# Performance work log

Hardware: AMD Instinct MI355X
Metric: run time of the kernel (lower is better)

Reference implementation:

```python
import jax, jax.numpy as jnp
import numpy as np

B, T, D, M, L = 4, 2048, 256, 128, 16
P = M * L  # max_pair_cnt


def setup_inputs() -> dict:
    key = jax.random.key(0)
    ks = jax.random.split(key, 11)
    head = jax.random.normal(ks[0], (B, P, T), jnp.float32) * 0.05
    tail = jax.random.normal(ks[1], (B, P, T), jnp.float32) * 0.05
    x = jax.random.normal(ks[2], (B, T, D), jnp.float32)
    coref_mention_position = jax.random.uniform(ks[3], (B, M, T), jnp.float32)
    lab = jax.random.uniform(ks[4], (B, P, 2), jnp.float32) + 1e-3
    coref_label = lab / lab.sum(-1, keepdims=True)  # already-softmaxed target
    coref_label_mask = jax.random.randint(ks[5], (B, P), 0, 2).astype(bool)
    lens = jnp.full((B, M), L, jnp.int32)  # uniform segment lengths
    w1 = jax.random.normal(ks[6], (3 * D, D), jnp.float32) / np.sqrt(3 * D).astype(np.float32)
    b1 = jnp.zeros((D,), jnp.float32)
    w2 = jax.random.normal(ks[7], (D, 2), jnp.float32) / np.sqrt(D).astype(np.float32)
    b2 = jnp.zeros((2,), jnp.float32)
    return {"head": head, "tail": tail, "lens": lens, "x": x,
            "coref_mention_position": coref_mention_position,
            "coref_label": coref_label, "coref_label_mask": coref_label_mask,
            "w1": w1, "b1": b1, "w2": w2, "b2": b2}


def reference(head, tail, lens, x, coref_mention_position, coref_label,
              coref_label_mask, w1, b1, w2, b2):
    # bmm-based gather of mention reps: [B,P,T] @ [B,T,D] -> [B,P,D]
    head_rep = jnp.einsum('bpt,btd->bpd', head, x)
    tail_rep = jnp.einsum('bpt,btd->bpd', tail, x)
    feat = jnp.concatenate([head_rep, tail_rep, head_rep * tail_rep], axis=-1)
    logits = jax.nn.relu(feat @ w1 + b1) @ w2 + b2  # [B,P,2]

    # ragged split_n_pad -> per-mention top-1 select (uniform lens == L -> reshape)
    scores = logits[..., 1].reshape(B, M, L)            # [B,M,L]
    max_idx = jnp.argmax(scores, axis=-1)               # [B,M]
    max_val = jnp.max(scores, axis=-1)                  # [B,M] (raw logit, as in source)
    tail_seg = tail_rep.reshape(B, M, L, D)
    sel = jnp.take_along_axis(tail_seg, max_idx[:, :, None, None], axis=2)[:, :, 0, :]
    coref_rep_m = sel * max_val[:, :, None]             # [B,M,D]

    # scatter-bmm merge back into sequence: [B,T,M] @ [B,M,D] -> [B,T,D]
    coref_rep = jnp.einsum('bmt,bmd->btd', coref_mention_position, coref_rep_m)
    output = x + coref_rep

    # KLDivLoss(reduction='mean') over masked pairs
    logq = jax.nn.log_softmax(logits, axis=-1)
    lab = coref_label
    pw = jnp.where(lab > 0, lab * jnp.log(jnp.maximum(lab, 1e-38)), 0.0) - lab * logq
    n = jnp.sum(coref_label_mask).astype(jnp.float32)
    loss = jnp.where(coref_label_mask[..., None], pw, 0.0).sum() / (n * 2.0)
    return output, loss
```

## Files before the change

### kernel.cpp

```cpp
#include <hip/hip_runtime.h>
#include <hip/hip_bf16.h>
#include <stdint.h>

#define TAU 0.05f

typedef __attribute__((ext_vector_type(8))) _Float16 f16x8;
typedef __attribute__((ext_vector_type(4))) float f32x4;

__device__ __forceinline__ unsigned short f2h(float f) {
  _Float16 h = (_Float16)f;
  return __builtin_bit_cast(unsigned short, h);
}
__device__ __forceinline__ void async_copy16(const void* g, void* l) {
  __builtin_amdgcn_global_load_lds(
      (const __attribute__((address_space(1))) unsigned int*)g,
      (__attribute__((address_space(3))) unsigned int*)l, 16, 0, 0);
}

__global__ __launch_bounds__(256) void k_prep(
    const float* __restrict__ x, const float* __restrict__ w1,
    const float* __restrict__ b2,
    unsigned short* __restrict__ xt, unsigned short* __restrict__ w1t,
    float* __restrict__ logits, int* __restrict__ njobs) {
  __shared__ float tileS[64][65];
  int bx = blockIdx.x, tid = threadIdx.x;
  if (bx == 0 && tid == 0) *njobs = 0;
  if (bx < 64) {
    int i = bx * 256 + tid;
    logits[i] = b2[i & 1];
  }
  int j = tid & 63, i0 = tid >> 6;
  if (bx < 512) {
    int b = bx >> 7, t6 = (bx >> 2) & 31, d6 = bx & 3;
    const float* src = x + ((size_t)b * 2048 + (size_t)t6 * 64) * 256 + d6 * 64;
    for (int i = i0; i < 64; i += 4) tileS[i][j] = src[(size_t)i * 256 + j];
    __syncthreads();
    unsigned short* dst = xt + ((size_t)b * 256 + (size_t)d6 * 64) * 2048 + t6 * 64;
    for (int r = i0; r < 64; r += 4) dst[(size_t)r * 2048 + j] = f2h(tileS[j][r]);
  } else {
    int wt = bx - 512;
    int k6 = wt >> 2, n6 = wt & 3;
    const float* src = w1 + ((size_t)k6 * 64) * 256 + n6 * 64;
    for (int i = i0; i < 64; i += 4) tileS[i][j] = src[(size_t)i * 256 + j];
    __syncthreads();
    unsigned short* dst = w1t + ((size_t)n6 * 64) * 768 + k6 * 64;
    for (int r = i0; r < 64; r += 4) dst[(size_t)r * 768 + j] = f2h(tileS[j][r]);
  }
}

__global__ __launch_bounds__(1024, 1) void k_gemm_rep(
    const float* __restrict__ head, const float* __restrict__ tail,
    const unsigned short* __restrict__ xt,
    float* __restrict__ hrep, float* __restrict__ trep) {
  __shared__ unsigned short Bs[2][32768];
  int bx = blockIdx.x;
  int isTail = bx >> 7;
  int g2 = bx & 127;
  int b = g2 >> 5;
  int rowt = (g2 & 31) * 64;
  const float* Asrc = (isTail ? tail : head) + ((size_t)(b * 2048 + rowt)) * 2048;
  float* Crep = isTail ? trep : hrep;
  const unsigned short* xtb = xt + (size_t)b * 256 * 2048;

  int tid = threadIdx.x, lane = tid & 63, w = tid >> 6;
  int l15 = lane & 15, l4 = lane >> 4;
  int msub = w & 3, nsub = w >> 2;
  const float* rowptr = Asrc + (size_t)(msub * 16 + l15) * 2048 + l4 * 8;

  f32x4 acc[4];
#pragma unroll
  for (int ct = 0; ct < 4; ++ct) acc[ct] = (f32x4){0.f, 0.f, 0.f, 0.f};

  float4 aw[8], af[8];

  auto stageB = [&](int iv, int buf) {
    int k0 = iv * 128;
#pragma unroll
    for (int q = 0; q < 4; ++q) {
      const unsigned short* src = xtb + (size_t)(q * 64 + lane) * 2048 + k0 + w * 8;
      async_copy16(src, &Bs[buf][(w * 256 + q * 64 + lane) * 8]);
    }
  };
  auto loadA = [&](float4* dst, int iv) {
    const float* p = rowptr + iv * 128;
#pragma unroll
    for (int s = 0; s < 4; ++s) {
      dst[2 * s] = *(const float4*)(p + s * 32);
      dst[2 * s + 1] = *(const float4*)(p + s * 32 + 4);
    }
  };

  stageB(0, 0);
  loadA(aw, 0);
  __syncthreads();

  for (int iv = 0; iv < 16; ++iv) {
    int cur = iv & 1, nxt = cur ^ 1;
    if (iv < 15) {
      stageB(iv + 1, nxt);
      loadA(af, iv + 1);
    }
    const unsigned short* B_ = Bs[cur];
#pragma unroll
    for (int s = 0; s < 4; ++s) {
      f16x8 a;
      float4 u = aw[2 * s], v = aw[2 * s + 1];
      a[0] = (_Float16)u.x; a[1] = (_Float16)u.y;
      a[2] = (_Float16)u.z; a[3] = (_Float16)u.w;
      a[4] = (_Float16)v.x; a[5] = (_Float16)v.y;
      a[6] = (_Float16)v.z; a[7] = (_Float16)v.w;
#pragma unroll
      for (int ct = 0; ct < 4; ++ct) {
        f16x8 bf = *(const f16x8*)&B_[((s * 4 + l4) * 256 + nsub * 64 + ct * 16 + l15) * 8];
        acc[ct] = __builtin_amdgcn_mfma_f32_16x16x32_f16(a, bf, acc[ct], 0, 0, 0);
      }
    }
    if (iv < 15) {
#pragma unroll
      for (int r = 0; r < 8; ++r) aw[r] = af[r];
    }
    __syncthreads();
  }

  size_t grow = (size_t)b * 2048 + rowt + msub * 16 + l4 * 4;
  int gcol = nsub * 64 + l15;
#pragma unroll
  for (int ct = 0; ct < 4; ++ct)
#pragma unroll
    for (int i = 0; i < 4; ++i)
      Crep[(grow + i) * 256 + gcol + ct * 16] = acc[ct][i];
}

__global__ __launch_bounds__(256) void k_feat(
    const float* __restrict__ hrep, const float* __restrict__ trep,
    unsigned short* __restrict__ featf) {
  int gid = blockIdx.x * 256 + threadIdx.x;
  int p = gid >> 6, d0 = (gid & 63) * 4;
  float4 h4 = *(const float4*)&hrep[(size_t)p * 256 + d0];
  float4 t4 = *(const float4*)&trep[(size_t)p * 256 + d0];
  ushort4 a, bb, c;
  a.x = f2h(h4.x); a.y = f2h(h4.y); a.z = f2h(h4.z); a.w = f2h(h4.w);
  bb.x = f2h(t4.x); bb.y = f2h(t4.y); bb.z = f2h(t4.z); bb.w = f2h(t4.w);
  c.x = f2h(h4.x * t4.x); c.y = f2h(h4.y * t4.y);
  c.z = f2h(h4.z * t4.z); c.w = f2h(h4.w * t4.w);
  *(ushort4*)&featf[(size_t)p * 768 + d0] = a;
  *(ushort4*)&featf[(size_t)p * 768 + 256 + d0] = bb;
  *(ushort4*)&featf[(size_t)p * 768 + 512 + d0] = c;
}

__global__ __launch_bounds__(256) void k_gemm_mlp(
    const unsigned short* __restrict__ featf, const unsigned short* __restrict__ w1t,
    const float* __restrict__ b1, const float* __restrict__ w2,
    float* __restrict__ logits) {
  int bx = blockIdx.x;
  int mt = bx >> 2, nt = bx & 3;
  int tid = threadIdx.x, lane = tid & 63, w = tid >> 6;
  int l15 = lane & 15, l4 = lane >> 4;
  int wm = (w & 1) * 32, wn = (w >> 1) * 32;

  const unsigned short* arow[2];
  const unsigned short* brow[2];
#pragma unroll
  for (int j = 0; j < 2; ++j) {
    arow[j] = featf + (size_t)(mt * 64 + wm + j * 16 + l15) * 768 + l4 * 8;
    brow[j] = w1t + (size_t)(nt * 64 + wn + j * 16 + l15) * 768 + l4 * 8;
  }

  f32x4 acc[2][2];
#pragma unroll
  for (int jm = 0; jm < 2; ++jm)
#pragma unroll
    for (int jn = 0; jn < 2; ++jn) acc[jm][jn] = (f32x4){0.f, 0.f, 0.f, 0.f};

  f16x8 a_[2][2], b_[2][2];
#pragma unroll
  for (int p = 0; p < 2; ++p)
#pragma unroll
    for (int j = 0; j < 2; ++j) {
      a_[p][j] = *(const f16x8*)(arow[j] + p * 32);
      b_[p][j] = *(const f16x8*)(brow[j] + p * 32);
    }

  for (int s = 0; s < 24; ++s) {
    int c = s & 1;
    f16x8 ta0 = a_[c][0], ta1 = a_[c][1], tb0 = b_[c][0], tb1 = b_[c][1];
    if (s + 2 < 24) {
#pragma unroll
      for (int j = 0; j < 2; ++j) {
        a_[c][j] = *(const f16x8*)(arow[j] + (s + 2) * 32);
        b_[c][j] = *(const f16x8*)(brow[j] + (s + 2) * 32);
      }
    }
    acc[0][0] = __builtin_amdgcn_mfma_f32_16x16x32_f16(ta0, tb0, acc[0][0], 0, 0, 0);
    acc[0][1] = __builtin_amdgcn_mfma_f32_16x16x32_f16(ta0, tb1, acc[0][1], 0, 0, 0);
    acc[1][0] = __builtin_amdgcn_mfma_f32_16x16x32_f16(ta1, tb0, acc[1][0], 0, 0, 0);
    acc[1][1] = __builtin_amdgcn_mfma_f32_16x16x32_f16(ta1, tb1, acc[1][1], 0, 0, 0);
  }

  float bv[2], w20[2], w21[2];
#pragma unroll
  for (int jn = 0; jn < 2; ++jn) {
    int col = nt * 64 + wn + jn * 16 + l15;
    bv[jn] = b1[col]; w20[jn] = w2[col * 2]; w21[jn] = w2[col * 2 + 1];
  }
#pragma unroll
  for (int jm = 0; jm < 2; ++jm)
#pragma unroll
    for (int i = 0; i < 4; ++i) {
      float s0 = 0.f, s1 = 0.f;
#pragma unroll
      for (int jn = 0; jn < 2; ++jn) {
        float r = fmaxf(acc[jm][jn][i] + bv[jn], 0.f);
        s0 += r * w20[jn]; s1 += r * w21[jn];
      }
#pragma unroll
      for (int off = 1; off < 16; off <<= 1) {
        s0 += __shfl_xor(s0, off); s1 += __shfl_xor(s1, off);
      }
      if (l15 == 0) {
        int row = mt * 64 + wm + jm * 16 + l4 * 4 + i;
        atomicAdd(&logits[row * 2], s0);
        atomicAdd(&logits[row * 2 + 1], s1);
      }
    }
}

__global__ void k_select(const float* __restrict__ logits, int* __restrict__ idxv,
                         float* __restrict__ mval, int* __restrict__ cmask,
                         int* __restrict__ njobs, int* __restrict__ jobs) {
  int q = blockIdx.x * 256 + threadIdx.x;
  if (q >= 512) return;
  int base = q * 16;
  float s[16];
#pragma unroll
  for (int i = 0; i < 16; ++i) s[i] = logits[(size_t)(base + i) * 2 + 1];
  float best = s[0]; int bi = 0;
#pragma unroll
  for (int i = 1; i < 16; ++i) if (s[i] > best) { best = s[i]; bi = i; }
  int mask = 0, cnt = 0;
#pragma unroll
  for (int i = 0; i < 16; ++i) if (s[i] > best - TAU) { mask |= 1 << i; ++cnt; }
  idxv[q] = bi; mval[q] = best;
  if (cnt > 1) {
    cmask[q] = mask;
    for (int i = 0; i < 16; ++i)
      if ((mask >> i) & 1) { int j = atomicAdd(njobs, 1); jobs[j] = base + i; }
  } else cmask[q] = 0;
}

__global__ __launch_bounds__(1024) void k_refine(
    const int* __restrict__ njobs, const int* __restrict__ jobs,
    const float* __restrict__ head, const float* __restrict__ tail,
    const float* __restrict__ x, const float* __restrict__ w1,
    const float* __restrict__ b1, const float* __restrict__ w2,
    const float* __restrict__ b2, float* __restrict__ refined) {
  __shared__ float hrow[2048], trow[2048], feat[768], red[1024], red2[1024];
  int tid = threadIdx.x, seg = tid >> 8, d = tid & 255;
  int nj = *njobs;
  for (int job = blockIdx.x; job < nj; job += gridDim.x) {
    int code = jobs[job];
    int b = code >> 11, p = code & 2047;
    if (tid < 512)
      *(float4*)&hrow[tid * 4] = *(const float4*)&head[((size_t)(b * 2048 + p)) * 2048 + tid * 4];
    else {
      int u = tid - 512;
      *(float4*)&trow[u * 4] = *(const float4*)&tail[((size_t)(b * 2048 + p)) * 2048 + u * 4];
    }
    __syncthreads();
    float hr = 0.f, tr = 0.f;
    const float* xb = x + ((size_t)b * 2048) * 256 + d;
#pragma unroll 8
    for (int t = seg * 512; t < seg * 512 + 512; ++t) {
      float xv = xb[(size_t)t * 256];
      hr += hrow[t] * xv; tr += trow[t] * xv;
    }
    red[tid] = hr; red2[tid] = tr;
    __syncthreads();
    if (seg == 0) {
      float fh = red[d] + red[256 + d] + red[512 + d] + red[768 + d];
      float ft = red2[d] + red2[256 + d] + red2[512 + d] + red2[768 + d];
      feat[d] = fh; feat[256 + d] = ft; feat[512 + d] = fh * ft;
    }
    __syncthreads();
    float hp = 0.f;
    for (int ii = seg * 192; ii < seg * 192 + 192; ++ii) hp += feat[ii] * w1[(size_t)ii * 256 + d];
    red[tid] = hp;
    __syncthreads();
    if (seg == 0) {
      float hj = b1[d] + red[d] + red[256 + d] + red[512 + d] + red[768 + d];
      hj = fmaxf(hj, 0.f);
      red2[d] = hj * w2[d * 2 + 1];
    }
    __syncthreads();
    for (int s = 128; s > 0; s >>= 1) {
      if (tid < s) red2[tid] += red2[tid + s];
      __syncthreads();
    }
    if (tid == 0) refined[code] = red2[0] + b2[1];
    __syncthreads();
  }
}

__global__ __launch_bounds__(256) void k_repm(
    const int* __restrict__ idxv, const float* __restrict__ mval,
    const int* __restrict__ cmask, const float* __restrict__ refined,
    const float* __restrict__ trep, float* __restrict__ repm) {
  int q = blockIdx.x, d = threadIdx.x;
  int mask = cmask[q]; int bi; float v;
  if (mask) {
    bi = -1; v = -1e30f;
    for (int i = 0; i < 16; ++i)
      if ((mask >> i) & 1) { float s = refined[q * 16 + i]; if (s > v) { v = s; bi = i; } }
  } else { bi = idxv[q]; v = mval[q]; }
  repm[(size_t)q * 256 + d] = trep[((size_t)q * 16 + bi) * 256 + d] * v;
}

__global__ __launch_bounds__(256) void k_merge(
    const float* __restrict__ cmp, const float* __restrict__ repm,
    const float* __restrict__ x, float* __restrict__ out) {
  __shared__ float cl[128 * 16];
  int bx = blockIdx.x, b = bx >> 7, t0 = (bx & 127) * 16;
  int tid = threadIdx.x;
#pragma unroll
  for (int it = 0; it < 2; ++it) {
    int f = it * 256 + tid;
    int row = f >> 2, c4 = (f & 3) * 4;
    *(float4*)&cl[row * 16 + c4] =
        *(const float4*)&cmp[((size_t)(b * 128 + row)) * 2048 + t0 + c4];
  }
  __syncthreads();
  float acc[16];
#pragma unroll
  for (int i = 0; i < 16; ++i) acc[i] = 0.f;
  int d = tid;
  for (int m = 0; m < 128; ++m) {
    float rv = repm[(size_t)(b * 128 + m) * 256 + d];
    const float4* c4p = (const float4*)&cl[m * 16];
#pragma unroll
    for (int jj = 0; jj < 4; ++jj) {
      float4 c = c4p[jj];
      acc[jj * 4] += c.x * rv; acc[jj * 4 + 1] += c.y * rv;
      acc[jj * 4 + 2] += c.z * rv; acc[jj * 4 + 3] += c.w * rv;
    }
  }
  const float* xb = x + ((size_t)(b * 2048 + t0)) * 256 + d;
  float* ob = out + ((size_t)(b * 2048 + t0)) * 256 + d;
#pragma unroll
  for (int tt = 0; tt < 16; ++tt) ob[(size_t)tt * 256] = xb[(size_t)tt * 256] + acc[tt];
}

__global__ __launch_bounds__(1024) void k_loss(
    const float* __restrict__ logits, const float* __restrict__ lab,
    const unsigned char* __restrict__ mask, float* __restrict__ out_loss) {
  __shared__ float rs[1024], rc[1024];
  int tid = threadIdx.x;
  float sum = 0.f, cnt = 0.f;
  for (int p = tid; p < 8192; p += 1024) {
    float l0 = logits[(size_t)p * 2], l1 = logits[(size_t)p * 2 + 1];
    float a0 = lab[(size_t)p * 2], a1 = lab[(size_t)p * 2 + 1];
    float mx = fmaxf(l0, l1);
    float lse = mx + logf(expf(l0 - mx) + expf(l1 - mx));
    float pw = 0.f;
    if (a0 > 0.f) pw += a0 * logf(fmaxf(a0, 1e-38f));
    if (a1 > 0.f) pw += a1 * logf(fmaxf(a1, 1e-38f));
    pw -= a0 * (l0 - lse) + a1 * (l1 - lse);
    if (mask[p]) { sum += pw; cnt += 1.f; }
  }
  rs[tid] = sum; rc[tid] = cnt;
  __syncthreads();
  for (int s = 512; s > 0; s >>= 1) {
    if (tid < s) { rs[tid] += rs[tid + s]; rc[tid] += rc[tid + s]; }
    __syncthreads();
  }
  if (tid == 0) *out_loss = rs[0] / (rc[0] * 2.0f);
}

extern "C" void kernel_launch(void* const* d_in, const int* in_sizes, int n_in,
                              void* d_out, int out_size, void* d_ws, size_t ws_size,
                              hipStream_t stream) {
  (void)in_sizes; (void)n_in; (void)out_size; (void)ws_size;
  const float* head = (const float*)d_in[0];
  const float* tail = (const float*)d_in[1];
  const float* x = (const float*)d_in[3];
  const float* cmp = (const float*)d_in[4];
  const float* lab = (const float*)d_in[5];
  const unsigned char* lmask = (const unsigned char*)d_in[6];
  const float* w1 = (const float*)d_in[7];
  const float* b1 = (const float*)d_in[8];
  const float* w2 = (const float*)d_in[9];
  const float* b2 = (const float*)d_in[10];
  float* out = (float*)d_out;

  char* ws = (char*)d_ws;
  size_t off = 0;
  auto alloc = [&](size_t bytes) -> void* {
    void* p = ws + off; off += (bytes + 255) & ~(size_t)255; return p;
  };
  unsigned short* xt = (unsigned short*)alloc(4ull * 256 * 2048 * 2);
  unsigned short* w1t = (unsigned short*)alloc(256ull * 768 * 2);
  float* hrep = (float*)alloc(8192ull * 256 * 4);
  float* trep = (float*)alloc(8192ull * 256 * 4);
  unsigned short* featf = (unsigned short*)alloc(8192ull * 768 * 2);
  float* logits = (float*)alloc(8192ull * 2 * 4);
  float* refined = (float*)alloc(8192ull * 4);
  int* idxv = (int*)alloc(512 * 4);
  float* mvalv = (float*)alloc(512 * 4);
  int* cmaskv = (int*)alloc(512 * 4);
  int* njobs = (int*)alloc(256);
  int* jobs = (int*)alloc(8192 * 4);
  float* repm = (float*)alloc(512ull * 256 * 4);

  k_prep<<<560, 256, 0, stream>>>(x, w1, b2, xt, w1t, logits, njobs);
  k_gemm_rep<<<256, 1024, 0, stream>>>(head, tail, xt, hrep, trep);
  k_feat<<<2048, 256, 0, stream>>>(hrep, trep, featf);
  k_gemm_mlp<<<512, 256, 0, stream>>>(featf, w1t, b1, w2, logits);
  k_select<<<2, 256, 0, stream>>>(logits, idxv, mvalv, cmaskv, njobs, jobs);
  k_refine<<<256, 1024, 0, stream>>>(njobs, jobs, head, tail, x, w1, b1, w2, b2, refined);
  k_repm<<<512, 256, 0, stream>>>(idxv, mvalv, cmaskv, refined, trep, repm);
  k_merge<<<512, 256, 0, stream>>>(cmp, repm, x, out);
  k_loss<<<1, 1024, 0, stream>>>(logits, lab, lmask, out + 4ull * 2048 * 256);
}
```

Measured before the change: 340.6 us.

## Retile rep GEMM, store reps in fp16, LDS-stage MLP GEMM, batch refine jobs

The rep GEMM moves from 1024-thread blocks with a 256-wide N tile to 512-thread blocks with a 128-wide N tile. A is staged through swizzled LDS and occupancy rises to 4 blocks per CU. Head and tail reps are written in fp16 instead of fp32, and k_feat now only computes the product term, so concatenated feature writes are gone. The MLP GEMM reads its A operand directly from the three fp16 sources through double-buffered swizzled LDS. The refine kernel groups up to 8 jobs per batch so x and w1 loads are reused across jobs. Storing reps in fp16 could change the argmax selection and the products slightly.

```diff
diff --git a/kernel.cpp b/kernel.cpp
--- a/kernel.cpp
+++ b/kernel.cpp
@@ -10,6 +10,10 @@
 __device__ __forceinline__ unsigned short f2h(float f) {
   _Float16 h = (_Float16)f;
   return __builtin_bit_cast(unsigned short, h);
+}
+__device__ __forceinline__ float h2f(unsigned short u) {
+  _Float16 h = __builtin_bit_cast(_Float16, u);
+  return (float)h;
 }
 __device__ __forceinline__ void async_copy16(const void* g, void* l) {
   __builtin_amdgcn_global_load_lds(
@@ -21,10 +25,10 @@
     const float* __restrict__ x, const float* __restrict__ w1,
     const float* __restrict__ b2,
     unsigned short* __restrict__ xt, unsigned short* __restrict__ w1t,
-    float* __restrict__ logits, int* __restrict__ njobs) {
+    float* __restrict__ logits, int* __restrict__ njobsb) {
   __shared__ float tileS[64][65];
   int bx = blockIdx.x, tid = threadIdx.x;
-  if (bx == 0 && tid == 0) *njobs = 0;
+  if (bx == 0 && tid < 4) njobsb[tid] = 0;
   if (bx < 64) {
     int i = bx * 256 + tid;
     logits[i] = b2[i & 1];
@@ -48,188 +52,226 @@
   }
 }
 
-__global__ __launch_bounds__(1024, 1) void k_gemm_rep(
+__global__ __launch_bounds__(512, 4) void k_gemm_rep(
     const float* __restrict__ head, const float* __restrict__ tail,
     const unsigned short* __restrict__ xt,
-    float* __restrict__ hrep, float* __restrict__ trep) {
-  __shared__ unsigned short Bs[2][32768];
+    unsigned short* __restrict__ hrep16, unsigned short* __restrict__ trep16) {
+  __shared__ unsigned short As[2][4096];
+  __shared__ unsigned short Bs[2][8192];
   int bx = blockIdx.x;
-  int isTail = bx >> 7;
-  int g2 = bx & 127;
-  int b = g2 >> 5;
-  int rowt = (g2 & 31) * 64;
-  const float* Asrc = (isTail ? tail : head) + ((size_t)(b * 2048 + rowt)) * 2048;
-  float* Crep = isTail ? trep : hrep;
-  const unsigned short* xtb = xt + (size_t)b * 256 * 2048;
+  int rt = bx >> 1, ntile = bx & 1;
+  int g0 = rt * 64;
+  int isTail = g0 >> 13;
+  int local = g0 & 8191;
+  int b = local >> 11;
+  const float* Asrc = (isTail ? tail : head) + (size_t)local * 2048;
+  unsigned short* Crep = isTail ? trep16 : hrep16;
+  const unsigned short* Bsrc = xt + ((size_t)b * 256 + ntile * 128) * 2048;
 
   int tid = threadIdx.x, lane = tid & 63, w = tid >> 6;
   int l15 = lane & 15, l4 = lane >> 4;
   int msub = w & 3, nsub = w >> 2;
-  const float* rowptr = Asrc + (size_t)(msub * 16 + l15) * 2048 + l4 * 8;
+
+  int arow = 8 * w + (lane >> 3), aj = lane & 7;
+  const float* aptr = Asrc + (size_t)arow * 2048 + aj * 8;
+  int awc = (arow * 8 + (aj ^ (arow & 7))) * 8;
+
+  int acOf[2];
+#pragma unroll
+  for (int s = 0; s < 2; ++s) {
+    int row = msub * 16 + l15, k8 = s * 4 + l4;
+    acOf[s] = (row * 8 + (k8 ^ (row & 7))) * 8;
+  }
+  int bcOf[2][4];
+#pragma unroll
+  for (int s = 0; s < 2; ++s)
+#pragma unroll
+    for (int ct = 0; ct < 4; ++ct) {
+      int col = nsub * 64 + ct * 16 + l15, k8 = s * 4 + l4;
+      bcOf[s][ct] = (col * 8 + (k8 ^ (col & 7))) * 8;
+    }
+
+  auto stageB = [&](int iv, unsigned short* buf) {
+#pragma unroll
+    for (int a = 0; a < 2; ++a) {
+      int e = 2 * w + a;
+      int colofs = lane >> 3, j = lane & 7;
+      int col = e * 8 + colofs;
+      const unsigned short* src =
+          Bsrc + (size_t)col * 2048 + iv * 64 + (j ^ colofs) * 8;
+      async_copy16(src, buf + ((size_t)e * 64 + lane) * 8);
+    }
+  };
+  auto loadA = [&](float4* v, int iv) {
+    const float* p = aptr + iv * 64;
+    v[0] = *(const float4*)p;
+    v[1] = *(const float4*)(p + 4);
+  };
+  auto packA = [&](const float4* v, unsigned short* buf) {
+    f16x8 pk;
+    pk[0] = (_Float16)v[0].x; pk[1] = (_Float16)v[0].y;
+    pk[2] = (_Float16)v[0].z; pk[3] = (_Float16)v[0].w;
+    pk[4] = (_Float16)v[1].x; pk[5] = (_Float16)v[1].y;
+    pk[6] = (_Float16)v[1].z; pk[7] = (_Float16)v[1].w;
+    *(f16x8*)(buf + awc) = pk;
+  };
 
   f32x4 acc[4];
 #pragma unroll
   for (int ct = 0; ct < 4; ++ct) acc[ct] = (f32x4){0.f, 0.f, 0.f, 0.f};
 
-  float4 aw[8], af[8];
-
-  auto stageB = [&](int iv, int buf) {
-    int k0 = iv * 128;
-#pragma unroll
-    for (int q = 0; q < 4; ++q) {
-      const unsigned short* src = xtb + (size_t)(q * 64 + lane) * 2048 + k0 + w * 8;
-      async_copy16(src, &Bs[buf][(w * 256 + q * 64 + lane) * 8]);
-    }
-  };
-  auto loadA = [&](float4* dst, int iv) {
-    const float* p = rowptr + iv * 128;
-#pragma unroll
-    for (int s = 0; s < 4; ++s) {
-      dst[2 * s] = *(const float4*)(p + s * 32);
-      dst[2 * s + 1] = *(const float4*)(p + s * 32 + 4);
-    }
-  };
-
-  stageB(0, 0);
-  loadA(aw, 0);
+  float4 avW[2], avF[2];
+  loadA(avW, 0);
+  stageB(0, Bs[0]);
+  packA(avW, As[0]);
+  loadA(avW, 1);
   __syncthreads();
 
-  for (int iv = 0; iv < 16; ++iv) {
-    int cur = iv & 1, nxt = cur ^ 1;
-    if (iv < 15) {
-      stageB(iv + 1, nxt);
-      loadA(af, iv + 1);
-    }
-    const unsigned short* B_ = Bs[cur];
-#pragma unroll
-    for (int s = 0; s < 4; ++s) {
-      f16x8 a;
-      float4 u = aw[2 * s], v = aw[2 * s + 1];
-      a[0] = (_Float16)u.x; a[1] = (_Float16)u.y;
-      a[2] = (_Float16)u.z; a[3] = (_Float16)u.w;
-      a[4] = (_Float16)v.x; a[5] = (_Float16)v.y;
-      a[6] = (_Float16)v.z; a[7] = (_Float16)v.w;
+  for (int it = 0; it < 32; ++it) {
+    int cur = it & 1, nxt = cur ^ 1;
+    if (it < 31) stageB(it + 1, Bs[nxt]);
+    if (it < 30) loadA(avF, it + 2);
+#pragma unroll
+    for (int s = 0; s < 2; ++s) {
+      f16x8 a = *(const f16x8*)&As[cur][acOf[s]];
 #pragma unroll
       for (int ct = 0; ct < 4; ++ct) {
-        f16x8 bf = *(const f16x8*)&B_[((s * 4 + l4) * 256 + nsub * 64 + ct * 16 + l15) * 8];
+        f16x8 bf = *(const f16x8*)&Bs[cur][bcOf[s][ct]];
         acc[ct] = __builtin_amdgcn_mfma_f32_16x16x32_f16(a, bf, acc[ct], 0, 0, 0);
       }
     }
-    if (iv < 15) {
-#pragma unroll
-      for (int r = 0; r < 8; ++r) aw[r] = af[r];
-    }
-    __syncthreads();
-  }
-
-  size_t grow = (size_t)b * 2048 + rowt + msub * 16 + l4 * 4;
-  int gcol = nsub * 64 + l15;
+    if (it < 31) {
+      packA(avW, As[nxt]);
+      avW[0] = avF[0]; avW[1] = avF[1];
+    }
+    __syncthreads();
+  }
+
+  int rowb = local + msub * 16 + l4 * 4;
+  int colb = ntile * 128 + nsub * 64 + l15;
 #pragma unroll
   for (int ct = 0; ct < 4; ++ct)
 #pragma unroll
     for (int i = 0; i < 4; ++i)
-      Crep[(grow + i) * 256 + gcol + ct * 16] = acc[ct][i];
+      Crep[(size_t)(rowb + i) * 256 + colb + ct * 16] = f2h(acc[ct][i]);
 }
 
 __global__ __launch_bounds__(256) void k_feat(
-    const float* __restrict__ hrep, const float* __restrict__ trep,
-    unsigned short* __restrict__ featf) {
+    const unsigned short* __restrict__ hrep16,
+    const unsigned short* __restrict__ trep16,
+    unsigned short* __restrict__ featp) {
   int gid = blockIdx.x * 256 + threadIdx.x;
-  int p = gid >> 6, d0 = (gid & 63) * 4;
-  float4 h4 = *(const float4*)&hrep[(size_t)p * 256 + d0];
-  float4 t4 = *(const float4*)&trep[(size_t)p * 256 + d0];
-  ushort4 a, bb, c;
-  a.x = f2h(h4.x); a.y = f2h(h4.y); a.z = f2h(h4.z); a.w = f2h(h4.w);
-  bb.x = f2h(t4.x); bb.y = f2h(t4.y); bb.z = f2h(t4.z); bb.w = f2h(t4.w);
-  c.x = f2h(h4.x * t4.x); c.y = f2h(h4.y * t4.y);
-  c.z = f2h(h4.z * t4.z); c.w = f2h(h4.w * t4.w);
-  *(ushort4*)&featf[(size_t)p * 768 + d0] = a;
-  *(ushort4*)&featf[(size_t)p * 768 + 256 + d0] = bb;
-  *(ushort4*)&featf[(size_t)p * 768 + 512 + d0] = c;
-}
-
-__global__ __launch_bounds__(256) void k_gemm_mlp(
-    const unsigned short* __restrict__ featf, const unsigned short* __restrict__ w1t,
+  size_t o = (size_t)gid * 4;
+  ushort4 h4 = *(const ushort4*)&hrep16[o];
+  ushort4 t4 = *(const ushort4*)&trep16[o];
+  ushort4 c;
+  c.x = f2h(h2f(h4.x) * h2f(t4.x)); c.y = f2h(h2f(h4.y) * h2f(t4.y));
+  c.z = f2h(h2f(h4.z) * h2f(t4.z)); c.w = f2h(h2f(h4.w) * h2f(t4.w));
+  *(ushort4*)&featp[o] = c;
+}
+
+__global__ __launch_bounds__(512, 4) void k_gemm_mlp(
+    const unsigned short* __restrict__ hrep16,
+    const unsigned short* __restrict__ trep16,
+    const unsigned short* __restrict__ featp,
+    const unsigned short* __restrict__ w1t,
     const float* __restrict__ b1, const float* __restrict__ w2,
     float* __restrict__ logits) {
+  __shared__ unsigned short As[2][4096];
+  __shared__ unsigned short Bs[2][4096];
   int bx = blockIdx.x;
-  int mt = bx >> 2, nt = bx & 3;
+  int rt = bx >> 2, ntile = bx & 3;
+  int row0 = rt * 64;
   int tid = threadIdx.x, lane = tid & 63, w = tid >> 6;
   int l15 = lane & 15, l4 = lane >> 4;
-  int wm = (w & 1) * 32, wn = (w >> 1) * 32;
-
-  const unsigned short* arow[2];
-  const unsigned short* brow[2];
-#pragma unroll
-  for (int j = 0; j < 2; ++j) {
-    arow[j] = featf + (size_t)(mt * 64 + wm + j * 16 + l15) * 768 + l4 * 8;
-    brow[j] = w1t + (size_t)(nt * 64 + wn + j * 16 + l15) * 768 + l4 * 8;
-  }
-
-  f32x4 acc[2][2];
-#pragma unroll
-  for (int jm = 0; jm < 2; ++jm)
-#pragma unroll
-    for (int jn = 0; jn < 2; ++jn) acc[jm][jn] = (f32x4){0.f, 0.f, 0.f, 0.f};
-
-  f16x8 a_[2][2], b_[2][2];
-#pragma unroll
-  for (int p = 0; p < 2; ++p)
-#pragma unroll
-    for (int j = 0; j < 2; ++j) {
-      a_[p][j] = *(const f16x8*)(arow[j] + p * 32);
-      b_[p][j] = *(const f16x8*)(brow[j] + p * 32);
-    }
-
-  for (int s = 0; s < 24; ++s) {
-    int c = s & 1;
-    f16x8 ta0 = a_[c][0], ta1 = a_[c][1], tb0 = b_[c][0], tb1 = b_[c][1];
-    if (s + 2 < 24) {
-#pragma unroll
-      for (int j = 0; j < 2; ++j) {
-        a_[c][j] = *(const f16x8*)(arow[j] + (s + 2) * 32);
-        b_[c][j] = *(const f16x8*)(brow[j] + (s + 2) * 32);
+  int msub = w & 3, nsub = w >> 2;
+
+  int acOf[2];
+#pragma unroll
+  for (int s = 0; s < 2; ++s) {
+    int row = msub * 16 + l15, k8 = s * 4 + l4;
+    acOf[s] = (row * 8 + (k8 ^ (row & 7))) * 8;
+  }
+  int bcOf[2][2];
+#pragma unroll
+  for (int s = 0; s < 2; ++s)
+#pragma unroll
+    for (int ct = 0; ct < 2; ++ct) {
+      int col = nsub * 32 + ct * 16 + l15, k8 = s * 4 + l4;
+      bcOf[s][ct] = (col * 8 + (k8 ^ (col & 7))) * 8;
+    }
+
+  int rowofs = lane >> 3, j7 = lane & 7;
+  auto stageA = [&](int iv, unsigned short* buf) {
+    const unsigned short* s; int ko;
+    if (iv < 4)      { s = hrep16; ko = iv * 64; }
+    else if (iv < 8) { s = trep16; ko = (iv - 4) * 64; }
+    else             { s = featp;  ko = (iv - 8) * 64; }
+    const unsigned short* src =
+        s + (size_t)(row0 + w * 8 + rowofs) * 256 + ko + (j7 ^ rowofs) * 8;
+    async_copy16(src, buf + ((size_t)w * 64 + lane) * 8);
+  };
+  auto stageBm = [&](int iv, unsigned short* buf) {
+    const unsigned short* src =
+        w1t + (size_t)(ntile * 64 + w * 8 + rowofs) * 768 + iv * 64 + (j7 ^ rowofs) * 8;
+    async_copy16(src, buf + ((size_t)w * 64 + lane) * 8);
+  };
+
+  f32x4 acc[2];
+  acc[0] = (f32x4){0.f, 0.f, 0.f, 0.f};
+  acc[1] = (f32x4){0.f, 0.f, 0.f, 0.f};
+
+  stageA(0, As[0]);
+  stageBm(0, Bs[0]);
+  __syncthreads();
+
+  for (int it = 0; it < 12; ++it) {
+    int cur = it & 1, nxt = cur ^ 1;
+    if (it < 11) { stageA(it + 1, As[nxt]); stageBm(it + 1, Bs[nxt]); }
+#pragma unroll
+    for (int s = 0; s < 2; ++s) {
+      f16x8 a = *(const f16x8*)&As[cur][acOf[s]];
+#pragma unroll
+      for (int ct = 0; ct < 2; ++ct) {
+        f16x8 bf = *(const f16x8*)&Bs[cur][bcOf[s][ct]];
+        acc[ct] = __builtin_amdgcn_mfma_f32_16x16x32_f16(a, bf, acc[ct], 0, 0, 0);
       }
     }
-    acc[0][0] = __builtin_amdgcn_mfma_f32_16x16x32_f16(ta0, tb0, acc[0][0], 0, 0, 0);
-    acc[0][1] = __builtin_amdgcn_mfma_f32_16x16x32_f16(ta0, tb1, acc[0][1], 0, 0, 0);
-    acc[1][0] = __builtin_amdgcn_mfma_f32_16x16x32_f16(ta1, tb0, acc[1][0], 0, 0, 0);
-    acc[1][1] = __builtin_amdgcn_mfma_f32_16x16x32_f16(ta1, tb1, acc[1][1], 0, 0, 0);
+    __syncthreads();
   }
 
   float bv[2], w20[2], w21[2];
 #pragma unroll
-  for (int jn = 0; jn < 2; ++jn) {
-    int col = nt * 64 + wn + jn * 16 + l15;
-    bv[jn] = b1[col]; w20[jn] = w2[col * 2]; w21[jn] = w2[col * 2 + 1];
-  }
-#pragma unroll
-  for (int jm = 0; jm < 2; ++jm)
-#pragma unroll
-    for (int i = 0; i < 4; ++i) {
-      float s0 = 0.f, s1 = 0.f;
-#pragma unroll
-      for (int jn = 0; jn < 2; ++jn) {
-        float r = fmaxf(acc[jm][jn][i] + bv[jn], 0.f);
-        s0 += r * w20[jn]; s1 += r * w21[jn];
-      }
-#pragma unroll
-      for (int off = 1; off < 16; off <<= 1) {
-        s0 += __shfl_xor(s0, off); s1 += __shfl_xor(s1, off);
-      }
-      if (l15 == 0) {
-        int row = mt * 64 + wm + jm * 16 + l4 * 4 + i;
-        atomicAdd(&logits[row * 2], s0);
-        atomicAdd(&logits[row * 2 + 1], s1);
-      }
-    }
+  for (int ct = 0; ct < 2; ++ct) {
+    int col = ntile * 64 + nsub * 32 + ct * 16 + l15;
+    bv[ct] = b1[col]; w20[ct] = w2[col * 2]; w21[ct] = w2[col * 2 + 1];
+  }
+#pragma unroll
+  for (int i = 0; i < 4; ++i) {
+    float s0 = 0.f, s1 = 0.f;
+#pragma unroll
+    for (int ct = 0; ct < 2; ++ct) {
+      float r = fmaxf(acc[ct][i] + bv[ct], 0.f);
+      s0 += r * w20[ct]; s1 += r * w21[ct];
+    }
+#pragma unroll
+    for (int off = 1; off < 16; off <<= 1) {
+      s0 += __shfl_xor(s0, off); s1 += __shfl_xor(s1, off);
+    }
+    if (l15 == 0) {
+      int row = row0 + msub * 16 + l4 * 4 + i;
+      atomicAdd(&logits[row * 2], s0);
+      atomicAdd(&logits[row * 2 + 1], s1);
+    }
+  }
 }
 
 __global__ void k_select(const float* __restrict__ logits, int* __restrict__ idxv,
                          float* __restrict__ mval, int* __restrict__ cmask,
-                         int* __restrict__ njobs, int* __restrict__ jobs) {
+                         int* __restrict__ njobsb, int* __restrict__ jobsb) {
   int q = blockIdx.x * 256 + threadIdx.x;
   if (q >= 512) return;
+  int b = q >> 7;
   int base = q * 16;
   float s[16];
 #pragma unroll
@@ -244,67 +286,104 @@
   if (cnt > 1) {
     cmask[q] = mask;
     for (int i = 0; i < 16; ++i)
-      if ((mask >> i) & 1) { int j = atomicAdd(njobs, 1); jobs[j] = base + i; }
+      if ((mask >> i) & 1) {
+        int idx = atomicAdd(&njobsb[b], 1);
+        jobsb[b * 2048 + idx] = base + i;
+      }
   } else cmask[q] = 0;
 }
 
 __global__ __launch_bounds__(1024) void k_refine(
-    const int* __restrict__ njobs, const int* __restrict__ jobs,
+    const int* __restrict__ njobsb, const int* __restrict__ jobsb,
     const float* __restrict__ head, const float* __restrict__ tail,
     const float* __restrict__ x, const float* __restrict__ w1,
     const float* __restrict__ b1, const float* __restrict__ w2,
     const float* __restrict__ b2, float* __restrict__ refined) {
-  __shared__ float hrow[2048], trow[2048], feat[768], red[1024], red2[1024];
-  int tid = threadIdx.x, seg = tid >> 8, d = tid & 255;
-  int nj = *njobs;
-  for (int job = blockIdx.x; job < nj; job += gridDim.x) {
-    int code = jobs[job];
-    int b = code >> 11, p = code & 2047;
-    if (tid < 512)
-      *(float4*)&hrow[tid * 4] = *(const float4*)&head[((size_t)(b * 2048 + p)) * 2048 + tid * 4];
-    else {
-      int u = tid - 512;
-      *(float4*)&trow[u * 4] = *(const float4*)&tail[((size_t)(b * 2048 + p)) * 2048 + u * 4];
-    }
-    __syncthreads();
-    float hr = 0.f, tr = 0.f;
+  __shared__ float hT[2048 * 8];
+  __shared__ float tT[2048 * 8];
+  __shared__ float red[1024], red2[1024];
+  __shared__ int jc[8];
+  float* featL = hT;
+
+  int tid = threadIdx.x;
+  int d = tid & 255, seg = tid >> 8;
+  int nch[4], tot = 0;
+#pragma unroll
+  for (int b = 0; b < 4; ++b) { int n = njobsb[b]; nch[b] = (n + 7) >> 3; tot += nch[b]; }
+
+  for (int g = blockIdx.x; g < tot; g += gridDim.x) {
+    int b = 0, c = g;
+    while (c >= nch[b]) { c -= nch[b]; ++b; }
+    int nj = njobsb[b];
+    int j0 = c * 8, jn = min(8, nj - j0);
+    if (tid < 8) jc[tid] = (tid < jn) ? jobsb[b * 2048 + j0 + tid] : -1;
+    __syncthreads();
+    for (int j = 0; j < jn; ++j) {
+      int p = jc[j] & 2047;
+      const float* hr = head + ((size_t)(b * 2048 + p)) * 2048;
+      const float* tr = tail + ((size_t)(b * 2048 + p)) * 2048;
+      for (int t = tid; t < 2048; t += 1024) {
+        hT[t * 8 + j] = hr[t];
+        tT[t * 8 + j] = tr[t];
+      }
+    }
+    __syncthreads();
+    float ha[8], ta[8];
+#pragma unroll
+    for (int j = 0; j < 8; ++j) { ha[j] = 0.f; ta[j] = 0.f; }
     const float* xb = x + ((size_t)b * 2048) * 256 + d;
-#pragma unroll 8
     for (int t = seg * 512; t < seg * 512 + 512; ++t) {
       float xv = xb[(size_t)t * 256];
-      hr += hrow[t] * xv; tr += trow[t] * xv;
-    }
-    red[tid] = hr; red2[tid] = tr;
-    __syncthreads();
-    if (seg == 0) {
-      float fh = red[d] + red[256 + d] + red[512 + d] + red[768 + d];
-      float ft = red2[d] + red2[256 + d] + red2[512 + d] + red2[768 + d];
-      feat[d] = fh; feat[256 + d] = ft; feat[512 + d] = fh * ft;
-    }
-    __syncthreads();
-    float hp = 0.f;
-    for (int ii = seg * 192; ii < seg * 192 + 192; ++ii) hp += feat[ii] * w1[(size_t)ii * 256 + d];
-    red[tid] = hp;
-    __syncthreads();
-    if (seg == 0) {
-      float hj = b1[d] + red[d] + red[256 + d] + red[512 + d] + red[768 + d];
-      hj = fmaxf(hj, 0.f);
-      red2[d] = hj * w2[d * 2 + 1];
-    }
-    __syncthreads();
-    for (int s = 128; s > 0; s >>= 1) {
-      if (tid < s) red2[tid] += red2[tid + s];
+      float4 h0 = *(const float4*)&hT[t * 8], h1 = *(const float4*)&hT[t * 8 + 4];
+      float4 t0 = *(const float4*)&tT[t * 8], t1 = *(const float4*)&tT[t * 8 + 4];
+      ha[0] += h0.x * xv; ha[1] += h0.y * xv; ha[2] += h0.z * xv; ha[3] += h0.w * xv;
+      ha[4] += h1.x * xv; ha[5] += h1.y * xv; ha[6] += h1.z * xv; ha[7] += h1.w * xv;
+      ta[0] += t0.x * xv; ta[1] += t0.y * xv; ta[2] += t0.z * xv; ta[3] += t0.w * xv;
+      ta[4] += t1.x * xv; ta[5] += t1.y * xv; ta[6] += t1.z * xv; ta[7] += t1.w * xv;
+    }
+    __syncthreads();
+    for (int j = 0; j < jn; ++j) {
+      red[tid] = ha[j]; red2[tid] = ta[j];
       __syncthreads();
-    }
-    if (tid == 0) refined[code] = red2[0] + b2[1];
-    __syncthreads();
+      if (seg == 0) {
+        float fh = red[d] + red[256 + d] + red[512 + d] + red[768 + d];
+        float ft = red2[d] + red2[256 + d] + red2[512 + d] + red2[768 + d];
+        featL[j * 768 + d] = fh;
+        featL[j * 768 + 256 + d] = ft;
+        featL[j * 768 + 512 + d] = fh * ft;
+      }
+      __syncthreads();
+    }
+    float hacc[8];
+#pragma unroll
+    for (int j = 0; j < 8; ++j) hacc[j] = 0.f;
+    for (int ii = seg * 192; ii < seg * 192 + 192; ++ii) {
+      float wv = w1[(size_t)ii * 256 + d];
+#pragma unroll
+      for (int j = 0; j < 8; ++j) hacc[j] += featL[j * 768 + ii] * wv;
+    }
+    for (int j = 0; j < jn; ++j) {
+      red[tid] = hacc[j];
+      __syncthreads();
+      if (seg == 0) {
+        float h = b1[d] + red[d] + red[256 + d] + red[512 + d] + red[768 + d];
+        h = fmaxf(h, 0.f);
+        float v = h * w2[d * 2 + 1];
+        for (int off = 32; off; off >>= 1) v += __shfl_xor(v, off);
+        if ((tid & 63) == 0) red2[tid >> 6] = v;
+      }
+      __syncthreads();
+      if (tid == 0)
+        refined[jc[j]] = red2[0] + red2[1] + red2[2] + red2[3] + b2[1];
+      __syncthreads();
+    }
   }
 }
 
 __global__ __launch_bounds__(256) void k_repm(
     const int* __restrict__ idxv, const float* __restrict__ mval,
     const int* __restrict__ cmask, const float* __restrict__ refined,
-    const float* __restrict__ trep, float* __restrict__ repm) {
+    const unsigned short* __restrict__ trep16, float* __restrict__ repm) {
   int q = blockIdx.x, d = threadIdx.x;
   int mask = cmask[q]; int bi; float v;
   if (mask) {
@@ -312,7 +391,7 @@
     for (int i = 0; i < 16; ++i)
       if ((mask >> i) & 1) { float s = refined[q * 16 + i]; if (s > v) { v = s; bi = i; } }
   } else { bi = idxv[q]; v = mval[q]; }
-  repm[(size_t)q * 256 + d] = trep[((size_t)q * 16 + bi) * 256 + d] * v;
+  repm[(size_t)q * 256 + d] = h2f(trep16[((size_t)q * 16 + bi) * 256 + d]) * v;
 }
 
 __global__ __launch_bounds__(256) void k_merge(
@@ -398,25 +477,25 @@
   };
   unsigned short* xt = (unsigned short*)alloc(4ull * 256 * 2048 * 2);
   unsigned short* w1t = (unsigned short*)alloc(256ull * 768 * 2);
-  float* hrep = (float*)alloc(8192ull * 256 * 4);
-  float* trep = (float*)alloc(8192ull * 256 * 4);
-  unsigned short* featf = (unsigned short*)alloc(8192ull * 768 * 2);
+  unsigned short* hrep16 = (unsigned short*)alloc(8192ull * 256 * 2);
+  unsigned short* trep16 = (unsigned short*)alloc(8192ull * 256 * 2);
+  unsigned short* featp = (unsigned short*)alloc(8192ull * 256 * 2);
   float* logits = (float*)alloc(8192ull * 2 * 4);
   float* refined = (float*)alloc(8192ull * 4);
   int* idxv = (int*)alloc(512 * 4);
   float* mvalv = (float*)alloc(512 * 4);
   int* cmaskv = (int*)alloc(512 * 4);
-  int* njobs = (int*)alloc(256);
-  int* jobs = (int*)alloc(8192 * 4);
+  int* njobsb = (int*)alloc(256);
+  int* jobsb = (int*)alloc(4 * 2048 * 4);
   float* repm = (float*)alloc(512ull * 256 * 4);
 
-  k_prep<<<560, 256, 0, stream>>>(x, w1, b2, xt, w1t, logits, njobs);
-  k_gemm_rep<<<256, 1024, 0, stream>>>(head, tail, xt, hrep, trep);
-  k_feat<<<2048, 256, 0, stream>>>(hrep, trep, featf);
-  k_gemm_mlp<<<512, 256, 0, stream>>>(featf, w1t, b1, w2, logits);
-  k_select<<<2, 256, 0, stream>>>(logits, idxv, mvalv, cmaskv, njobs, jobs);
-  k_refine<<<256, 1024, 0, stream>>>(njobs, jobs, head, tail, x, w1, b1, w2, b2, refined);
-  k_repm<<<512, 256, 0, stream>>>(idxv, mvalv, cmaskv, refined, trep, repm);
+  k_prep<<<560, 256, 0, stream>>>(x, w1, b2, xt, w1t, logits, njobsb);
+  k_gemm_rep<<<512, 512, 0, stream>>>(head, tail, xt, hrep16, trep16);
+  k_feat<<<2048, 256, 0, stream>>>(hrep16, trep16, featp);
+  k_gemm_mlp<<<512, 512, 0, stream>>>(hrep16, trep16, featp, w1t, b1, w2, logits);
+  k_select<<<2, 256, 0, stream>>>(logits, idxv, mvalv, cmaskv, njobsb, jobsb);
+  k_refine<<<256, 1024, 0, stream>>>(njobsb, jobsb, head, tail, x, w1, b1, w2, b2, refined);
+  k_repm<<<512, 256, 0, stream>>>(idxv, mvalv, cmaskv, refined, trep16, repm);
   k_merge<<<512, 256, 0, stream>>>(cmp, repm, x, out);
   k_loss<<<1, 1024, 0, stream>>>(logits, lab, lmask, out + 4ull * 2048 * 256);
 }
```

New measurement: 363.3 us. 6.7% more time.
